# Optimization experiments

Measured on AMD Instinct MI355X. Metric: run time of the kernel, lower is better.

Reference implementation:

```python
import jax, jax.numpy as jnp
import numpy as np
import math

FS = 256
NUM_SHOT = 5


def pe_table(L, d=FS):
    pos = np.arange(L, dtype=np.float32)[:, None]
    div = np.exp(np.arange(0, d, 2, dtype=np.float32) * (-math.log(10000.0) / float(d)))
    pe = np.zeros((L, d), dtype=np.float32)
    pe[:, 0::2] = np.sin(pos * div)
    pe[:, 1::2] = np.cos(pos * div)
    return jnp.asarray(pe)


def _conv(x, w, b, stride=1):
    pad = [(1, 1), (1, 1)] if w.shape[2] == 3 else [(0, 0), (0, 0)]
    y = jax.lax.conv_general_dilated(x, w, (stride, stride), pad,
                                     dimension_numbers=('NCHW', 'OIHW', 'NCHW'))
    return y + b[None, :, None, None]


def _up2(x):
    return jnp.repeat(jnp.repeat(x, 2, axis=2), 2, axis=3)


def setup_inputs() -> dict:
    key = jax.random.key(0)
    ks = iter(jax.random.split(key, 40))
    n = lambda shape, s=0.02: jax.random.normal(next(ks), shape, dtype=jnp.float32) * s
    inp = {
        'C3': jax.random.normal(next(ks), (8, 512, 40, 40), dtype=jnp.float32),
        'C4': jax.random.normal(next(ks), (8, 1024, 20, 20), dtype=jnp.float32),
        'C5': jax.random.normal(next(ks), (8, 2048, 10, 10), dtype=jnp.float32),
        'S3': jax.random.normal(next(ks), (40, 512, 40, 40), dtype=jnp.float32),
        'S4': jax.random.normal(next(ks), (40, 1024, 20, 20), dtype=jnp.float32),
        'S5': jax.random.normal(next(ks), (40, 2048, 10, 10), dtype=jnp.float32),
        'w_p3_1': n((FS, 512, 1, 1)), 'b_p3_1': jnp.zeros((FS,), jnp.float32),
        'w_p3_2': n((FS, FS, 3, 3)), 'b_p3_2': jnp.zeros((FS,), jnp.float32),
        'w_p4_1': n((FS, 1024, 1, 1)), 'b_p4_1': jnp.zeros((FS,), jnp.float32),
        'w_p4_2': n((FS, FS, 3, 3)), 'b_p4_2': jnp.zeros((FS,), jnp.float32),
        'w_p5_1': n((FS, 2048, 1, 1)), 'b_p5_1': jnp.zeros((FS,), jnp.float32),
        'w_p5_2': n((FS, FS, 3, 3)), 'b_p5_2': jnp.zeros((FS,), jnp.float32),
        'w_p6': n((FS, 2048, 3, 3)), 'b_p6': jnp.zeros((FS,), jnp.float32),
        'w_p7': n((FS, FS, 3, 3)), 'b_p7': jnp.zeros((FS,), jnp.float32),
        'wq': n((FS, FS), 0.01), 'bq': jnp.zeros((FS,), jnp.float32),
        'wk': n((FS, FS), 0.01), 'bk': jnp.zeros((FS,), jnp.float32),
    }
    return inp


def reference(C3, C4, C5, S3, S4, S5,
              w_p3_1, b_p3_1, w_p3_2, b_p3_2,
              w_p4_1, b_p4_1, w_p4_2, b_p4_2,
              w_p5_1, b_p5_1, w_p5_2, b_p5_2,
              w_p6, b_p6, w_p7, b_p7, wq, bq, wk, bk):
    B = C3.shape[0]
    # lateral 1x1 convs (shared between query and support)
    P5x = _conv(C5, w_p5_1, b_p5_1)
    P4x = _conv(C4, w_p4_1, b_p4_1)
    P3x = _conv(C3, w_p3_1, b_p3_1)
    P5s = _conv(S5, w_p5_1, b_p5_1)
    P4s = _conv(S4, w_p4_1, b_p4_1)
    P3s = _conv(S3, w_p3_1, b_p3_1)
    # P6/P7 heads
    P6x = _conv(C5, w_p6, b_p6, stride=2)
    P7x = _conv(jax.nn.relu(P6x), w_p7, b_p7, stride=2)
    P6s = _conv(S5, w_p6, b_p6, stride=2)
    P7s = _conv(jax.nn.relu(P6s), w_p7, b_p7, stride=2)
    # query-side top-down FPN
    P4x = _up2(P5x) + P4x
    P5x2 = _conv(P5x, w_p5_2, b_p5_2)
    P3x = P3x + _up2(P4x)
    P4x2 = _conv(P4x, w_p4_2, b_p4_2)
    P3x2 = _conv(P3x, w_p3_2, b_p3_2)
    # support: [B*S, C, h, w] -> [S, B, C, h, w]
    split = lambda x: x.reshape(B, NUM_SHOT, x.shape[1], x.shape[2], x.shape[3]).transpose(1, 0, 2, 3, 4)
    q_feats = [P3x2, P4x2, P5x2, P6x, P7x]
    s_feats = [split(P3s), split(P4s), split(P5s), split(P6s), split(P7s)]
    pes = [pe_table(h * w) for h, w in [(40, 40), (20, 20), (10, 10), (5, 5), (3, 3)]]
    scale = 1.0 / math.sqrt(float(FS))
    outs = []
    for qx, sx, pe in zip(q_feats, s_feats, pes):
        _, C, H, W = qx.shape
        q = qx.reshape(B, C, H * W).transpose(0, 2, 1)                       # [B, L, C]
        s = sx.reshape(NUM_SHOT, B, C, H * W).transpose(0, 1, 3, 2) + pe      # [S, B, L, C]
        Q = q @ wq.T + bq
        K = s @ wk.T + bk
        scores = jnp.einsum('blc,sbmc->sblm', Q, K) * scale                   # [S, B, L, L]
        A = jax.nn.softmax(scores, axis=-1)
        out = jnp.einsum('sblm,sbmc->blc', A, s) / NUM_SHOT                   # shot mean
        m = out.transpose(0, 2, 1).reshape(B, C, H, W)
        outs.append(jnp.concatenate([qx, m], axis=1))
    return tuple(outs)
```

## Files before the change

kernel.cpp:

```cpp
#include <hip/hip_runtime.h>

typedef unsigned short u16;
typedef __attribute__((ext_vector_type(8))) short short8;
typedef __attribute__((ext_vector_type(4))) float floatx4;

#define DEV static __device__ __forceinline__

DEV u16 f2bf(float f) {
    union { float f; unsigned u; } v; v.f = f;
    unsigned r = v.u + 0x7fff + ((v.u >> 16) & 1);
    return (u16)(r >> 16);
}
DEV float bf2f(u16 h) {
    union { unsigned u; float f; } v; v.u = ((unsigned)h) << 16;
    return v.f;
}

DEV void load_lds16(const u16* g, u16* l) {
    __builtin_amdgcn_global_load_lds(
        (const __attribute__((address_space(1))) void*)g,
        (__attribute__((address_space(3))) void*)l, 16, 0, 0);
}

#define FLAG_BF16 1
#define FLAG_CF   2
#define FLAG_AT   4

__global__ __launch_bounds__(256, 2) void gemm_nt(
    const u16* __restrict__ A, const u16* __restrict__ BT,
    const float* __restrict__ bias,
    u16* __restrict__ obf, float* __restrict__ ocf, float* __restrict__ oat,
    int M, int K, int KS, int flags, int HW,
    long sA, long sBF, long sCF, long sAT)
{
    __shared__ u16 Al[4096];
    __shared__ u16 Bl[4096];
    const int tid = threadIdx.x, lane = tid & 63, w = tid >> 6;
    const int wr = w & 1, wc = w >> 1;
    const int col16 = lane & 15, quad = (lane >> 4) & 3;
    const int mt = blockIdx.x, nt = blockIdx.y & 1, ks = blockIdx.y >> 1, z = blockIdx.z;
    const int m0 = mt * 128, n0 = nt * 128;
    const u16* Ab = A + (size_t)z * sA;
    const int Kper = K / KS;
    const int kbeg = ks * Kper;
    const floatx4 fz = {0.f, 0.f, 0.f, 0.f};

    floatx4 acc[4][4];
#pragma unroll
    for (int i = 0; i < 4; ++i)
#pragma unroll
        for (int j = 0; j < 4; ++j) acc[i][j] = fz;

    for (int kb = 0; kb < Kper; kb += 32) {
        const int k0 = kbeg + kb;
        __syncthreads();
#pragma unroll
        for (int i = 0; i < 2; ++i) {
            int cc = w * 2 + i;
            int q = cc >> 1;
            int row = (cc & 1) * 64 + lane;
            int rg = m0 + row; rg = rg < M ? rg : (M - 1);
            load_lds16(Ab + (size_t)rg * K + k0 + q * 8, &Al[cc * 512]);
            int nr = n0 + row;
            load_lds16(BT + (size_t)nr * K + k0 + q * 8, &Bl[cc * 512]);
        }
        __syncthreads();
        short8 af[4], bfr[4];
#pragma unroll
        for (int i = 0; i < 4; ++i)
            af[i] = *(const short8*)&Al[(quad * 128 + wr * 64 + i * 16 + col16) * 8];
#pragma unroll
        for (int j = 0; j < 4; ++j)
            bfr[j] = *(const short8*)&Bl[(quad * 128 + wc * 64 + j * 16 + col16) * 8];
#pragma unroll
        for (int i = 0; i < 4; ++i)
#pragma unroll
            for (int j = 0; j < 4; ++j)
                acc[i][j] = __builtin_amdgcn_mfma_f32_16x16x32_bf16(af[i], bfr[j], acc[i][j], 0, 0, 0);
    }

#pragma unroll
    for (int j = 0; j < 4; ++j) {
        int gcol = n0 + wc * 64 + j * 16 + col16;
        float bv = (ks == 0) ? bias[gcol] : 0.f;
#pragma unroll
        for (int i = 0; i < 4; ++i) {
            int rowb = m0 + wr * 64 + i * 16 + quad * 4;
#pragma unroll
            for (int r = 0; r < 4; ++r) {
                int row = rowb + r;
                if (row < M) {
                    float v = acc[i][j][r] + bv;
                    if (flags & FLAG_BF16) obf[(size_t)z * sBF + (size_t)row * 256 + gcol] = f2bf(v);
                    if (flags & FLAG_CF)   ocf[(size_t)z * sCF + (size_t)gcol * HW + row] = v;
                    if (flags & FLAG_AT)   atomicAdd(&oat[(size_t)z * sAT + (size_t)row * 256 + gcol], v);
                }
            }
        }
    }
}

__global__ __launch_bounds__(256, 2) void flash_attn(
    const u16* __restrict__ Q,
    const u16* __restrict__ K,
    const u16* __restrict__ VT,
    float* __restrict__ outp, int L)
{
    __shared__ u16 Kl[8192];
    __shared__ u16 Vt[8192];
    __shared__ u16 Pl[4096];
    __shared__ float lrun[128];
    const int tid = threadIdx.x, lane = tid & 63, w = tid >> 6;
    const int col16 = lane & 15, quad = (lane >> 4) & 3;
    const int b = blockIdx.z, sh = blockIdx.y, sb = b * 5 + sh;
    const int q0 = blockIdx.x * 128;
    const u16* Qb = Q + (size_t)b * L * 256;
    const u16* Kb = K + (size_t)sb * L * 256;
    const u16* Vb = VT + (size_t)sb * 256 * L;
    const floatx4 fz = {0.f, 0.f, 0.f, 0.f};

    short8 qf[2][8];
#pragma unroll
    for (int lt = 0; lt < 2; ++lt) {
        int row = q0 + w * 32 + lt * 16 + col16; row = row < L ? row : (L - 1);
#pragma unroll
        for (int kc = 0; kc < 8; ++kc)
            qf[lt][kc] = *(const short8*)(Qb + (size_t)row * 256 + kc * 32 + quad * 8);
    }

    floatx4 acc[8][4];
#pragma unroll
    for (int lr = 0; lr < 8; ++lr)
#pragma unroll
        for (int ct = 0; ct < 4; ++ct) acc[lr][ct] = fz;
    float rsum[2][4] = {{0.f,0.f,0.f,0.f},{0.f,0.f,0.f,0.f}};

    const int nkt = (L + 31) >> 5;
    for (int kt = 0; kt < nkt; ++kt) {
        __syncthreads();
#pragma unroll
        for (int i = 0; i < 4; ++i) {
            int cc = w * 4 + i;
            int cg = cc * 2 + (lane >> 5);
            int row = lane & 31;
            int rg = kt * 32 + row; rg = rg < L ? rg : (L - 1);
            load_lds16(Kb + (size_t)rg * 256 + cg * 8, &Kl[cc * 512]);
            int c = cc * 16 + (lane >> 2);
            int m0 = (lane & 3) * 8;
            load_lds16(Vb + (size_t)c * L + kt * 32 + m0, &Vt[cc * 512]);
        }
        __syncthreads();
        floatx4 s00 = fz, s01 = fz, s10 = fz, s11 = fz;
#pragma unroll
        for (int kc = 0; kc < 8; ++kc) {
            short8 b0 = *(const short8*)&Kl[((kc * 4 + quad) * 32 + col16) * 8];
            short8 b1 = *(const short8*)&Kl[((kc * 4 + quad) * 32 + 16 + col16) * 8];
            s00 = __builtin_amdgcn_mfma_f32_16x16x32_bf16(qf[0][kc], b0, s00, 0, 0, 0);
            s01 = __builtin_amdgcn_mfma_f32_16x16x32_bf16(qf[0][kc], b1, s01, 0, 0, 0);
            s10 = __builtin_amdgcn_mfma_f32_16x16x32_bf16(qf[1][kc], b0, s10, 0, 0, 0);
            s11 = __builtin_amdgcn_mfma_f32_16x16x32_bf16(qf[1][kc], b1, s11, 0, 0, 0);
        }
        const bool v0 = (kt * 32 + col16) < L;
        const bool v1 = (kt * 32 + 16 + col16) < L;
        float p0[4], p1[4], p2[4], p3[4];
#pragma unroll
        for (int r = 0; r < 4; ++r) {
            p0[r] = v0 ? __expf(s00[r] * 0.0625f) : 0.f;
            p1[r] = v1 ? __expf(s01[r] * 0.0625f) : 0.f;
            p2[r] = v0 ? __expf(s10[r] * 0.0625f) : 0.f;
            p3[r] = v1 ? __expf(s11[r] * 0.0625f) : 0.f;
        }
#pragma unroll
        for (int r = 0; r < 4; ++r) {
            float v = p0[r] + p1[r];
            v += __shfl_xor(v, 1); v += __shfl_xor(v, 2); v += __shfl_xor(v, 4); v += __shfl_xor(v, 8);
            rsum[0][r] += v;
            float u = p2[r] + p3[r];
            u += __shfl_xor(u, 1); u += __shfl_xor(u, 2); u += __shfl_xor(u, 4); u += __shfl_xor(u, 8);
            rsum[1][r] += u;
        }
#pragma unroll
        for (int r = 0; r < 4; ++r) {
            int l0 = w * 32 + quad * 4 + r;
            Pl[l0 * 32 + col16]        = f2bf(p0[r]);
            Pl[l0 * 32 + 16 + col16]   = f2bf(p1[r]);
            Pl[(l0 + 16) * 32 + col16]      = f2bf(p2[r]);
            Pl[(l0 + 16) * 32 + 16 + col16] = f2bf(p3[r]);
        }
        __syncthreads();
#pragma unroll
        for (int ct = 0; ct < 4; ++ct) {
            short8 bv = *(const short8*)&Vt[(w * 64 + ct * 16 + col16) * 32 + quad * 8];
#pragma unroll
            for (int lr = 0; lr < 8; ++lr) {
                short8 ap = *(const short8*)&Pl[(lr * 16 + col16) * 32 + quad * 8];
                acc[lr][ct] = __builtin_amdgcn_mfma_f32_16x16x32_bf16(ap, bv, acc[lr][ct], 0, 0, 0);
            }
        }
    }

    if (col16 == 0) {
#pragma unroll
        for (int lt = 0; lt < 2; ++lt)
#pragma unroll
            for (int r = 0; r < 4; ++r) lrun[w * 32 + lt * 16 + quad * 4 + r] = rsum[lt][r];
    }
    __syncthreads();

#pragma unroll
    for (int lr = 0; lr < 8; ++lr) {
#pragma unroll
        for (int r = 0; r < 4; ++r) {
            int lloc = lr * 16 + quad * 4 + r;
            int l = q0 + lloc;
            if (l < L) {
                float sc = 0.2f / lrun[lloc];
#pragma unroll
                for (int ct = 0; ct < 4; ++ct) {
                    int c = w * 64 + ct * 16 + col16;
                    atomicAdd(&outp[((size_t)b * 512 + 256 + c) * L + l], acc[lr][ct][r] * sc);
                }
            }
        }
    }
}


__global__ void transp_cast(const float* __restrict__ in, u16* __restrict__ out, int C, int HW) {
    __shared__ float t[32][33];
    int z = blockIdx.z;
    int p0 = blockIdx.x * 32, c0 = blockIdx.y * 32;
    int tx = threadIdx.x & 31, ty = threadIdx.x >> 5;
    const float* ib = in + (size_t)z * C * HW;
    u16* ob = out + (size_t)z * HW * C;
#pragma unroll
    for (int i = 0; i < 4; ++i) {
        int c = c0 + ty + i * 8, p = p0 + tx;
        t[ty + i * 8][tx] = (p < HW) ? ib[(size_t)c * HW + p] : 0.f;
    }
    __syncthreads();
#pragma unroll
    for (int i = 0; i < 4; ++i) {
        int p = p0 + ty + i * 8, c = c0 + tx;
        if (p < HW) ob[(size_t)p * C + c] = f2bf(t[tx][ty + i * 8]);
    }
}

__global__ void transp_bf(const u16* __restrict__ in, u16* __restrict__ out, int L) {
    __shared__ u16 t[32][33];
    int z = blockIdx.z;
    int l0 = blockIdx.x * 32, c0 = blockIdx.y * 32;
    int tx = threadIdx.x & 31, ty = threadIdx.x >> 5;
    const u16* ib = in + (size_t)z * L * 256;
    u16* ob = out + (size_t)z * 256 * L;
#pragma unroll
    for (int i = 0; i < 4; ++i) {
        int l = l0 + ty + i * 8;
        t[ty + i * 8][tx] = (l < L) ? ib[(size_t)l * 256 + c0 + tx] : (u16)0;
    }
    __syncthreads();
#pragma unroll
    for (int i = 0; i < 4; ++i) {
        int l = l0 + tx, c = c0 + ty + i * 8;
        if (l < L) ob[(size_t)c * L + l] = t[tx][ty + i * 8];
    }
}

__global__ void cast1d(const float* __restrict__ in, u16* __restrict__ out, long n) {
    long i = (long)blockIdx.x * 256 + threadIdx.x;
    if (i < n) out[i] = f2bf(in[i]);
}

__global__ void reorder_w3(const float* __restrict__ in, u16* __restrict__ out, int C) {
    long i = (long)blockIdx.x * 256 + threadIdx.x;
    int co = (int)(i / (9L * C));
    int r = (int)(i % (9L * C));
    int t = r / C, c = r % C;
    out[i] = f2bf(in[((size_t)co * C + c) * 9 + t]);
}

__global__ void im2col_s1(const u16* __restrict__ in, u16* __restrict__ out, int H, int Wd) {
    int z = blockIdx.y, p = blockIdx.x, c = threadIdx.x;
    int y = p / Wd, x = p % Wd;
    const u16* ib = in + (size_t)z * H * Wd * 256;
    u16* ob = out + ((size_t)z * H * Wd + p) * 2304;
#pragma unroll
    for (int t = 0; t < 9; ++t) {
        int ys = y + t / 3 - 1, xs = x + t % 3 - 1;
        u16 v = 0;
        if (ys >= 0 && ys < H && xs >= 0 && xs < Wd) v = ib[((size_t)ys * Wd + xs) * 256 + c];
        ob[t * 256 + c] = v;
    }
}

__global__ void im2col_s2(const u16* __restrict__ in, u16* __restrict__ out,
                          int Hin, int Win, int Hout, int Wout, int C, int relu) {
    int z = blockIdx.y, p = blockIdx.x, tid = threadIdx.x;
    int oy = p / Wout, ox = p % Wout;
    const u16* ib = in + (size_t)z * Hin * Win * C;
    u16* ob = out + ((size_t)z * Hout * Wout + p) * (9L * C);
    for (int t = 0; t < 9; ++t) {
        int ys = oy * 2 + t / 3 - 1, xs = ox * 2 + t % 3 - 1;
        bool ok = (ys >= 0 && ys < Hin && xs >= 0 && xs < Win);
        for (int c = tid; c < C; c += 256) {
            u16 v = 0;
            if (ok) {
                v = ib[((size_t)ys * Win + xs) * C + c];
                if (relu && (v & 0x8000)) v = 0;
            }
            ob[(size_t)t * C + c] = v;
        }
    }
}

__global__ void up2add(u16* __restrict__ big, const u16* __restrict__ small, int Hb, int Wb) {
    int z = blockIdx.y, p = blockIdx.x, c = threadIdx.x;
    int y = p / Wb, x = p % Wb;
    size_t bi = ((size_t)z * Hb * Wb + p) * 256 + c;
    size_t si = ((size_t)z * (Hb / 2) * (Wb / 2) + (size_t)(y >> 1) * (Wb / 2) + (x >> 1)) * 256 + c;
    big[bi] = f2bf(bf2f(big[bi]) + bf2f(small[si]));
}

__global__ void add_pe(u16* __restrict__ s, int L) {
    int z = blockIdx.y, l = blockIdx.x, c = threadIdx.x;
    size_t i = ((size_t)z * L + l) * 256 + c;
    float arg = (float)l * expf(-0.035977892078031971f * (float)(c & ~1));
    float pe = (c & 1) ? cosf(arg) : sinf(arg);
    s[i] = f2bf(bf2f(s[i]) + pe);
}

__global__ void cast_cl(const float* __restrict__ in, u16* __restrict__ outbf,
                        float* __restrict__ doutcf, int M, int writecf) {
    int z = blockIdx.y, p = blockIdx.x, c = threadIdx.x;
    float v = in[((size_t)z * M + p) * 256 + c];
    outbf[((size_t)z * M + p) * 256 + c] = f2bf(v);
    if (writecf) doutcf[(size_t)z * 512 * M + (size_t)c * M + p] = v;
}

extern "C" void kernel_launch(void* const* d_in, const int* in_sizes, int n_in,
                              void* d_out, int out_size, void* d_ws, size_t ws_size,
                              hipStream_t stream)
{
    (void)in_sizes; (void)n_in;
    const float* C3 = (const float*)d_in[0];
    const float* C4 = (const float*)d_in[1];
    const float* C5 = (const float*)d_in[2];
    const float* S3 = (const float*)d_in[3];
    const float* S4 = (const float*)d_in[4];
    const float* S5 = (const float*)d_in[5];
    const float* w31 = (const float*)d_in[6];  const float* b31 = (const float*)d_in[7];
    const float* w32 = (const float*)d_in[8];  const float* b32 = (const float*)d_in[9];
    const float* w41 = (const float*)d_in[10]; const float* b41 = (const float*)d_in[11];
    const float* w42 = (const float*)d_in[12]; const float* b42 = (const float*)d_in[13];
    const float* w51 = (const float*)d_in[14]; const float* b51 = (const float*)d_in[15];
    const float* w52 = (const float*)d_in[16]; const float* b52 = (const float*)d_in[17];
    const float* w6  = (const float*)d_in[18]; const float* b6  = (const float*)d_in[19];
    const float* w7  = (const float*)d_in[20]; const float* b7  = (const float*)d_in[21];
    const float* wq  = (const float*)d_in[22]; const float* bq  = (const float*)d_in[23];
    const float* wk  = (const float*)d_in[24]; const float* bk  = (const float*)d_in[25];
    float* out = (float*)d_out;

    char* base = (char*)d_ws;
    size_t off = 0;
    auto alloc = [&](size_t bytes) -> void* {
        void* r = base + off;
        off = (off + bytes + 255) & ~(size_t)255;
        return r;
    };

    u16* X5t = (u16*)alloc((size_t)8  * 100  * 2048 * 2);
    u16* S5t = (u16*)alloc((size_t)40 * 100  * 2048 * 2);
    size_t alias_off = off;
    u16* X3t = (u16*)alloc((size_t)8  * 1600 * 512  * 2);
    u16* X4t = (u16*)alloc((size_t)8  * 400  * 1024 * 2);
    u16* S3t = (u16*)alloc((size_t)40 * 1600 * 512  * 2);
    u16* S4t = (u16*)alloc((size_t)40 * 400  * 1024 * 2);
    u16* imcol = (u16*)(base + alias_off);

    u16* w31b = (u16*)alloc(256L * 512 * 2);
    u16* w41b = (u16*)alloc(256L * 1024 * 2);
    u16* w51b = (u16*)alloc(256L * 2048 * 2);
    u16* wqb  = (u16*)alloc(256L * 256 * 2);
    u16* wkb  = (u16*)alloc(256L * 256 * 2);
    u16* w32b = (u16*)alloc(256L * 9 * 256 * 2);
    u16* w42b = (u16*)alloc(256L * 9 * 256 * 2);
    u16* w52b = (u16*)alloc(256L * 9 * 256 * 2);
    u16* w6b  = (u16*)alloc(256L * 9 * 2048 * 2);
    u16* w7b  = (u16*)alloc(256L * 9 * 256 * 2);

    u16* P3x = (u16*)alloc((size_t)8  * 1600 * 256 * 2);
    u16* P4x = (u16*)alloc((size_t)8  * 400  * 256 * 2);
    u16* P5x = (u16*)alloc((size_t)8  * 100  * 256 * 2);
    u16* P3s = (u16*)alloc((size_t)40 * 1600 * 256 * 2);
    u16* P4s = (u16*)alloc((size_t)40 * 400  * 256 * 2);
    u16* P5s = (u16*)alloc((size_t)40 * 100  * 256 * 2);
    u16* q3  = (u16*)alloc((size_t)8 * 1600 * 256 * 2);
    u16* q4  = (u16*)alloc((size_t)8 * 400  * 256 * 2);
    u16* q5  = (u16*)alloc((size_t)8 * 100  * 256 * 2);
    u16* q6  = (u16*)alloc((size_t)8 * 25   * 256 * 2);
    u16* q7  = (u16*)alloc((size_t)8 * 9    * 256 * 2);
    u16* P6sb = (u16*)alloc((size_t)40 * 25 * 256 * 2);
    u16* P7sb = (u16*)alloc((size_t)40 * 9  * 256 * 2);
    float* P6xf = (float*)alloc((size_t)8  * 25 * 256 * 4);
    float* P6sf = (float*)alloc((size_t)40 * 25 * 256 * 4);
    float* P7xf = (float*)alloc((size_t)8  * 9  * 256 * 4);
    float* P7sf = (float*)alloc((size_t)40 * 9  * 256 * 4);
    u16* Qb = (u16*)alloc((size_t)8  * 1600 * 256 * 2);
    u16* Kb = (u16*)alloc((size_t)40 * 1600 * 256 * 2);
    u16* sPeT = (u16*)alloc((size_t)40 * 256 * 1600 * 2 + 4096);

    if (off > ws_size) return;

    hipMemsetAsync(d_out, 0, (size_t)out_size * 4, stream);
    hipMemsetAsync(P6xf, 0, (size_t)8  * 25 * 256 * 4, stream);
    hipMemsetAsync(P6sf, 0, (size_t)40 * 25 * 256 * 4, stream);
    hipMemsetAsync(P7xf, 0, (size_t)8  * 9  * 256 * 4, stream);
    hipMemsetAsync(P7sf, 0, (size_t)40 * 9  * 256 * 4, stream);

    cast1d<<<dim3(512),  256, 0, stream>>>(w31, w31b, 256L * 512);
    cast1d<<<dim3(1024), 256, 0, stream>>>(w41, w41b, 256L * 1024);
    cast1d<<<dim3(2048), 256, 0, stream>>>(w51, w51b, 256L * 2048);
    cast1d<<<dim3(256),  256, 0, stream>>>(wq, wqb, 256L * 256);
    cast1d<<<dim3(256),  256, 0, stream>>>(wk, wkb, 256L * 256);
    reorder_w3<<<dim3(2304),  256, 0, stream>>>(w32, w32b, 256);
    reorder_w3<<<dim3(2304),  256, 0, stream>>>(w42, w42b, 256);
    reorder_w3<<<dim3(2304),  256, 0, stream>>>(w52, w52b, 256);
    reorder_w3<<<dim3(18432), 256, 0, stream>>>(w6, w6b, 2048);
    reorder_w3<<<dim3(2304),  256, 0, stream>>>(w7, w7b, 256);

    transp_cast<<<dim3(50, 16, 8),  256, 0, stream>>>(C3, X3t, 512, 1600);
    transp_cast<<<dim3(13, 32, 8),  256, 0, stream>>>(C4, X4t, 1024, 400);
    transp_cast<<<dim3(4,  64, 8),  256, 0, stream>>>(C5, X5t, 2048, 100);
    transp_cast<<<dim3(50, 16, 40), 256, 0, stream>>>(S3, S3t, 512, 1600);
    transp_cast<<<dim3(13, 32, 40), 256, 0, stream>>>(S4, S4t, 1024, 400);
    transp_cast<<<dim3(4,  64, 40), 256, 0, stream>>>(S5, S5t, 2048, 100);

    auto gemm = [&](const u16* A, const u16* BT, const float* bias,
                    u16* obf, float* ocf, float* oat,
                    int M, int K, int KS, int flags, int HW,
                    long sA, long sBF, long sCF, long sAT, int nb) {
        dim3 g((unsigned)((M + 127) / 128), (unsigned)(2 * KS), (unsigned)nb);
        gemm_nt<<<g, 256, 0, stream>>>(A, BT, bias, obf, ocf, oat, M, K, KS, flags, HW, sA, sBF, sCF, sAT);
    };

    gemm(X3t, w31b, b31, P3x, 0, 0, 1600, 512,  1, FLAG_BF16, 0, 1600L * 512,  1600L * 256, 0, 0, 8);
    gemm(X4t, w41b, b41, P4x, 0, 0, 400,  1024, 1, FLAG_BF16, 0, 400L * 1024,  400L * 256,  0, 0, 8);
    gemm(X5t, w51b, b51, P5x, 0, 0, 100,  2048, 1, FLAG_BF16, 0, 100L * 2048,  100L * 256,  0, 0, 8);
    gemm(S3t, w31b, b31, P3s, 0, 0, 1600, 512,  1, FLAG_BF16, 0, 1600L * 512,  1600L * 256, 0, 0, 40);
    gemm(S4t, w41b, b41, P4s, 0, 0, 400,  1024, 1, FLAG_BF16, 0, 400L * 1024,  400L * 256,  0, 0, 40);
    gemm(S5t, w51b, b51, P5s, 0, 0, 100,  2048, 1, FLAG_BF16, 0, 100L * 2048,  100L * 256,  0, 0, 40);

    const size_t lvl_off[5] = {0, 6553600, 8192000, 8601600, 8704000};

    im2col_s2<<<dim3(25, 8), 256, 0, stream>>>(X5t, imcol, 10, 10, 5, 5, 2048, 0);
    gemm(imcol, w6b, b6, 0, 0, P6xf, 25, 18432, 8, FLAG_AT, 0, 25L * 18432, 0, 0, 25L * 256, 8);
    im2col_s2<<<dim3(25, 40), 256, 0, stream>>>(S5t, imcol, 10, 10, 5, 5, 2048, 0);
    gemm(imcol, w6b, b6, 0, 0, P6sf, 25, 18432, 8, FLAG_AT, 0, 25L * 18432, 0, 0, 25L * 256, 40);
    cast_cl<<<dim3(25, 8),  256, 0, stream>>>(P6xf, q6, out + lvl_off[3], 25, 1);
    cast_cl<<<dim3(25, 40), 256, 0, stream>>>(P6sf, P6sb, 0, 25, 0);
    im2col_s2<<<dim3(9, 8), 256, 0, stream>>>(q6, imcol, 5, 5, 3, 3, 256, 1);
    gemm(imcol, w7b, b7, 0, 0, P7xf, 9, 2304, 4, FLAG_AT, 0, 9L * 2304, 0, 0, 9L * 256, 8);
    im2col_s2<<<dim3(9, 40), 256, 0, stream>>>(P6sb, imcol, 5, 5, 3, 3, 256, 1);
    gemm(imcol, w7b, b7, 0, 0, P7sf, 9, 2304, 4, FLAG_AT, 0, 9L * 2304, 0, 0, 9L * 256, 40);
    cast_cl<<<dim3(9, 8),  256, 0, stream>>>(P7xf, q7, out + lvl_off[4], 9, 1);
    cast_cl<<<dim3(9, 40), 256, 0, stream>>>(P7sf, P7sb, 0, 9, 0);

    up2add<<<dim3(400, 8),  256, 0, stream>>>(P4x, P5x, 20, 20);
    up2add<<<dim3(1600, 8), 256, 0, stream>>>(P3x, P4x, 40, 40);

    im2col_s1<<<dim3(100, 8), 256, 0, stream>>>(P5x, imcol, 10, 10);
    gemm(imcol, w52b, b52, q5, out + lvl_off[2], 0, 100, 2304, 1, FLAG_BF16 | FLAG_CF, 100,
         100L * 2304, 100L * 256, 512L * 100, 0, 8);
    im2col_s1<<<dim3(400, 8), 256, 0, stream>>>(P4x, imcol, 20, 20);
    gemm(imcol, w42b, b42, q4, out + lvl_off[1], 0, 400, 2304, 1, FLAG_BF16 | FLAG_CF, 400,
         400L * 2304, 400L * 256, 512L * 400, 0, 8);
    im2col_s1<<<dim3(1600, 8), 256, 0, stream>>>(P3x, imcol, 40, 40);
    gemm(imcol, w32b, b32, q3, out + lvl_off[0], 0, 1600, 2304, 1, FLAG_BF16 | FLAG_CF, 1600,
         1600L * 2304, 1600L * 256, 512L * 1600, 0, 8);

    const int Ls[5] = {1600, 400, 100, 25, 9};
    u16* qbuf[5] = {q3, q4, q5, q6, q7};
    u16* sbuf[5] = {P3s, P4s, P5s, P6sb, P7sb};
    for (int lv = 0; lv < 5; ++lv) {
        int L = Ls[lv];
        add_pe<<<dim3(L, 40), 256, 0, stream>>>(sbuf[lv], L);
        transp_bf<<<dim3((L + 31) / 32, 8, 40), 256, 0, stream>>>(sbuf[lv], sPeT, L);
        gemm(qbuf[lv], wqb, bq, Qb, 0, 0, L, 256, 1, FLAG_BF16, 0, (long)L * 256, (long)L * 256, 0, 0, 8);
        gemm(sbuf[lv], wkb, bk, Kb, 0, 0, L, 256, 1, FLAG_BF16, 0, (long)L * 256, (long)L * 256, 0, 0, 40);
        flash_attn<<<dim3((L + 127) / 128, 5, 8), 256, 0, stream>>>(Qb, Kb, sPeT, out + lvl_off[lv], L);
    }
}
```

Measured before the change: 2.333 ms.

## Replace fused flash attention with materialized exp-score GEMMs and batched flat GEMMs

```diff
diff --git a/kernel.cpp b/kernel.cpp
--- a/kernel.cpp
+++ b/kernel.cpp
@@ -23,15 +23,15 @@
 }
 
 #define FLAG_BF16 1
-#define FLAG_CF   2
 #define FLAG_AT   4
+#define FLAG_PV   8
 
 __global__ __launch_bounds__(256, 2) void gemm_nt(
     const u16* __restrict__ A, const u16* __restrict__ BT,
     const float* __restrict__ bias,
-    u16* __restrict__ obf, float* __restrict__ ocf, float* __restrict__ oat,
-    int M, int K, int KS, int flags, int HW,
-    long sA, long sBF, long sCF, long sAT)
+    u16* __restrict__ obf, float* __restrict__ oat, const float* __restrict__ lsum,
+    int M, int K, int KS, int flags, int zoff,
+    long sA, long sBT, long sBF, long sAT)
 {
     __shared__ u16 Al[4096];
     __shared__ u16 Bl[4096];
@@ -39,8 +39,10 @@
     const int wr = w & 1, wc = w >> 1;
     const int col16 = lane & 15, quad = (lane >> 4) & 3;
     const int mt = blockIdx.x, nt = blockIdx.y & 1, ks = blockIdx.y >> 1, z = blockIdx.z;
+    const int sb = zoff + z;
     const int m0 = mt * 128, n0 = nt * 128;
     const u16* Ab = A + (size_t)z * sA;
+    const u16* Bb = BT + (size_t)sb * sBT;
     const int Kper = K / KS;
     const int kbeg = ks * Kper;
     const floatx4 fz = {0.f, 0.f, 0.f, 0.f};
@@ -62,7 +64,7 @@
             int rg = m0 + row; rg = rg < M ? rg : (M - 1);
             load_lds16(Ab + (size_t)rg * K + k0 + q * 8, &Al[cc * 512]);
             int nr = n0 + row;
-            load_lds16(BT + (size_t)nr * K + k0 + q * 8, &Bl[cc * 512]);
+            load_lds16(Bb + (size_t)nr * K + k0 + q * 8, &Bl[cc * 512]);
         }
         __syncthreads();
         short8 af[4], bfr[4];
@@ -82,7 +84,7 @@
 #pragma unroll
     for (int j = 0; j < 4; ++j) {
         int gcol = n0 + wc * 64 + j * 16 + col16;
-        float bv = (ks == 0) ? bias[gcol] : 0.f;
+        float bv = (bias && ks == 0) ? bias[gcol] : 0.f;
 #pragma unroll
         for (int i = 0; i < 4; ++i) {
             int rowb = m0 + wr * 64 + i * 16 + quad * 4;
@@ -92,135 +94,88 @@
                 if (row < M) {
                     float v = acc[i][j][r] + bv;
                     if (flags & FLAG_BF16) obf[(size_t)z * sBF + (size_t)row * 256 + gcol] = f2bf(v);
-                    if (flags & FLAG_CF)   ocf[(size_t)z * sCF + (size_t)gcol * HW + row] = v;
                     if (flags & FLAG_AT)   atomicAdd(&oat[(size_t)z * sAT + (size_t)row * 256 + gcol], v);
+                    if (flags & FLAG_PV) {
+                        int bl = z / 5;
+                        float sc = 0.2f / lsum[(size_t)sb * 1664 + row];
+                        atomicAdd(&oat[(size_t)bl * sAT + (size_t)row * 256 + gcol], v * sc);
+                    }
                 }
             }
         }
     }
 }
 
-__global__ __launch_bounds__(256, 2) void flash_attn(
-    const u16* __restrict__ Q,
-    const u16* __restrict__ K,
-    const u16* __restrict__ VT,
-    float* __restrict__ outp, int L)
+__global__ __launch_bounds__(256, 2) void gemm_qk_exp(
+    const u16* __restrict__ Q, const u16* __restrict__ Km,
+    u16* __restrict__ eS, float* __restrict__ lsum,
+    int M, int Kpad, int zoff)
 {
-    __shared__ u16 Kl[8192];
-    __shared__ u16 Vt[8192];
-    __shared__ u16 Pl[4096];
-    __shared__ float lrun[128];
+    __shared__ u16 Al[4096];
+    __shared__ u16 Bl[4096];
     const int tid = threadIdx.x, lane = tid & 63, w = tid >> 6;
+    const int wr = w & 1, wc = w >> 1;
     const int col16 = lane & 15, quad = (lane >> 4) & 3;
-    const int b = blockIdx.z, sh = blockIdx.y, sb = b * 5 + sh;
-    const int q0 = blockIdx.x * 128;
-    const u16* Qb = Q + (size_t)b * L * 256;
-    const u16* Kb = K + (size_t)sb * L * 256;
-    const u16* Vb = VT + (size_t)sb * 256 * L;
+    const int mt = blockIdx.x, nt = blockIdx.y, z = blockIdx.z;
+    const int sb = zoff + z;
+    const int m0 = mt * 128, n0 = nt * 128;
+    const u16* Ab = Q + (size_t)(sb / 5) * M * 256;
+    const u16* Bb = Km + (size_t)sb * M * 256;
+    u16* eSb = eS + (size_t)z * M * Kpad;
     const floatx4 fz = {0.f, 0.f, 0.f, 0.f};
 
-    short8 qf[2][8];
-#pragma unroll
-    for (int lt = 0; lt < 2; ++lt) {
-        int row = q0 + w * 32 + lt * 16 + col16; row = row < L ? row : (L - 1);
-#pragma unroll
-        for (int kc = 0; kc < 8; ++kc)
-            qf[lt][kc] = *(const short8*)(Qb + (size_t)row * 256 + kc * 32 + quad * 8);
-    }
-
-    floatx4 acc[8][4];
-#pragma unroll
-    for (int lr = 0; lr < 8; ++lr)
-#pragma unroll
-        for (int ct = 0; ct < 4; ++ct) acc[lr][ct] = fz;
-    float rsum[2][4] = {{0.f,0.f,0.f,0.f},{0.f,0.f,0.f,0.f}};
-
-    const int nkt = (L + 31) >> 5;
-    for (int kt = 0; kt < nkt; ++kt) {
+    floatx4 acc[4][4];
+#pragma unroll
+    for (int i = 0; i < 4; ++i)
+#pragma unroll
+        for (int j = 0; j < 4; ++j) acc[i][j] = fz;
+
+    for (int k0 = 0; k0 < 256; k0 += 32) {
         __syncthreads();
 #pragma unroll
-        for (int i = 0; i < 4; ++i) {
-            int cc = w * 4 + i;
-            int cg = cc * 2 + (lane >> 5);
-            int row = lane & 31;
-            int rg = kt * 32 + row; rg = rg < L ? rg : (L - 1);
-            load_lds16(Kb + (size_t)rg * 256 + cg * 8, &Kl[cc * 512]);
-            int c = cc * 16 + (lane >> 2);
-            int m0 = (lane & 3) * 8;
-            load_lds16(Vb + (size_t)c * L + kt * 32 + m0, &Vt[cc * 512]);
+        for (int i = 0; i < 2; ++i) {
+            int cc = w * 2 + i;
+            int q = cc >> 1;
+            int row = (cc & 1) * 64 + lane;
+            int rg = m0 + row; rg = rg < M ? rg : (M - 1);
+            load_lds16(Ab + (size_t)rg * 256 + k0 + q * 8, &Al[cc * 512]);
+            int nr = n0 + row; nr = nr < M ? nr : (M - 1);
+            load_lds16(Bb + (size_t)nr * 256 + k0 + q * 8, &Bl[cc * 512]);
         }
         __syncthreads();
-        floatx4 s00 = fz, s01 = fz, s10 = fz, s11 = fz;
-#pragma unroll
-        for (int kc = 0; kc < 8; ++kc) {
-            short8 b0 = *(const short8*)&Kl[((kc * 4 + quad) * 32 + col16) * 8];
-            short8 b1 = *(const short8*)&Kl[((kc * 4 + quad) * 32 + 16 + col16) * 8];
-            s00 = __builtin_amdgcn_mfma_f32_16x16x32_bf16(qf[0][kc], b0, s00, 0, 0, 0);
-            s01 = __builtin_amdgcn_mfma_f32_16x16x32_bf16(qf[0][kc], b1, s01, 0, 0, 0);
-            s10 = __builtin_amdgcn_mfma_f32_16x16x32_bf16(qf[1][kc], b0, s10, 0, 0, 0);
-            s11 = __builtin_amdgcn_mfma_f32_16x16x32_bf16(qf[1][kc], b1, s11, 0, 0, 0);
-        }
-        const bool v0 = (kt * 32 + col16) < L;
-        const bool v1 = (kt * 32 + 16 + col16) < L;
-        float p0[4], p1[4], p2[4], p3[4];
+        short8 af[4], bfr[4];
+#pragma unroll
+        for (int i = 0; i < 4; ++i)
+            af[i] = *(const short8*)&Al[(quad * 128 + wr * 64 + i * 16 + col16) * 8];
+#pragma unroll
+        for (int j = 0; j < 4; ++j)
+            bfr[j] = *(const short8*)&Bl[(quad * 128 + wc * 64 + j * 16 + col16) * 8];
+#pragma unroll
+        for (int i = 0; i < 4; ++i)
+#pragma unroll
+            for (int j = 0; j < 4; ++j)
+                acc[i][j] = __builtin_amdgcn_mfma_f32_16x16x32_bf16(af[i], bfr[j], acc[i][j], 0, 0, 0);
+    }
+
+#pragma unroll
+    for (int i = 0; i < 4; ++i) {
 #pragma unroll
         for (int r = 0; r < 4; ++r) {
-            p0[r] = v0 ? __expf(s00[r] * 0.0625f) : 0.f;
-            p1[r] = v1 ? __expf(s01[r] * 0.0625f) : 0.f;
-            p2[r] = v0 ? __expf(s10[r] * 0.0625f) : 0.f;
-            p3[r] = v1 ? __expf(s11[r] * 0.0625f) : 0.f;
-        }
-#pragma unroll
-        for (int r = 0; r < 4; ++r) {
-            float v = p0[r] + p1[r];
-            v += __shfl_xor(v, 1); v += __shfl_xor(v, 2); v += __shfl_xor(v, 4); v += __shfl_xor(v, 8);
-            rsum[0][r] += v;
-            float u = p2[r] + p3[r];
-            u += __shfl_xor(u, 1); u += __shfl_xor(u, 2); u += __shfl_xor(u, 4); u += __shfl_xor(u, 8);
-            rsum[1][r] += u;
-        }
-#pragma unroll
-        for (int r = 0; r < 4; ++r) {
-            int l0 = w * 32 + quad * 4 + r;
-            Pl[l0 * 32 + col16]        = f2bf(p0[r]);
-            Pl[l0 * 32 + 16 + col16]   = f2bf(p1[r]);
-            Pl[(l0 + 16) * 32 + col16]      = f2bf(p2[r]);
-            Pl[(l0 + 16) * 32 + 16 + col16] = f2bf(p3[r]);
-        }
-        __syncthreads();
-#pragma unroll
-        for (int ct = 0; ct < 4; ++ct) {
-            short8 bv = *(const short8*)&Vt[(w * 64 + ct * 16 + col16) * 32 + quad * 8];
-#pragma unroll
-            for (int lr = 0; lr < 8; ++lr) {
-                short8 ap = *(const short8*)&Pl[(lr * 16 + col16) * 32 + quad * 8];
-                acc[lr][ct] = __builtin_amdgcn_mfma_f32_16x16x32_bf16(ap, bv, acc[lr][ct], 0, 0, 0);
+            int row = m0 + wr * 64 + i * 16 + quad * 4 + r;
+            float s = 0.f;
+#pragma unroll
+            for (int j = 0; j < 4; ++j) {
+                int gcol = n0 + wc * 64 + j * 16 + col16;
+                float v = 0.f;
+                if (row < M && gcol < M) v = __expf(acc[i][j][r] * 0.0625f);
+                u16 h = f2bf(v);
+                if (row < M) eSb[(size_t)row * Kpad + gcol] = h;
+                s += bf2f(h);
             }
-        }
-    }
-
-    if (col16 == 0) {
-#pragma unroll
-        for (int lt = 0; lt < 2; ++lt)
-#pragma unroll
-            for (int r = 0; r < 4; ++r) lrun[w * 32 + lt * 16 + quad * 4 + r] = rsum[lt][r];
-    }
-    __syncthreads();
-
-#pragma unroll
-    for (int lr = 0; lr < 8; ++lr) {
-#pragma unroll
-        for (int r = 0; r < 4; ++r) {
-            int lloc = lr * 16 + quad * 4 + r;
-            int l = q0 + lloc;
-            if (l < L) {
-                float sc = 0.2f / lrun[lloc];
-#pragma unroll
-                for (int ct = 0; ct < 4; ++ct) {
-                    int c = w * 64 + ct * 16 + col16;
-                    atomicAdd(&outp[((size_t)b * 512 + 256 + c) * L + l], acc[lr][ct][r] * sc);
-                }
-            }
+            s += __shfl_xor(s, 1); s += __shfl_xor(s, 2);
+            s += __shfl_xor(s, 4); s += __shfl_xor(s, 8);
+            if ((lane & 15) == 0 && row < M)
+                atomicAdd(&lsum[(size_t)sb * 1664 + row], s);
         }
     }
 }
@@ -246,13 +201,13 @@
     }
 }
 
-__global__ void transp_bf(const u16* __restrict__ in, u16* __restrict__ out, int L) {
+__global__ void transp_bf(const u16* __restrict__ in, u16* __restrict__ out, int L, int Kpad) {
     __shared__ u16 t[32][33];
     int z = blockIdx.z;
     int l0 = blockIdx.x * 32, c0 = blockIdx.y * 32;
     int tx = threadIdx.x & 31, ty = threadIdx.x >> 5;
     const u16* ib = in + (size_t)z * L * 256;
-    u16* ob = out + (size_t)z * 256 * L;
+    u16* ob = out + (size_t)z * 256 * Kpad;
 #pragma unroll
     for (int i = 0; i < 4; ++i) {
         int l = l0 + ty + i * 8;
@@ -262,7 +217,7 @@
 #pragma unroll
     for (int i = 0; i < 4; ++i) {
         int l = l0 + tx, c = c0 + ty + i * 8;
-        if (l < L) ob[(size_t)c * L + l] = t[tx][ty + i * 8];
+        ob[(size_t)c * Kpad + l] = t[tx][ty + i * 8];
     }
 }
 
@@ -329,12 +284,27 @@
     s[i] = f2bf(bf2f(s[i]) + pe);
 }
 
-__global__ void cast_cl(const float* __restrict__ in, u16* __restrict__ outbf,
-                        float* __restrict__ doutcf, int M, int writecf) {
-    int z = blockIdx.y, p = blockIdx.x, c = threadIdx.x;
-    float v = in[((size_t)z * M + p) * 256 + c];
-    outbf[((size_t)z * M + p) * 256 + c] = f2bf(v);
-    if (writecf) doutcf[(size_t)z * 512 * M + (size_t)c * M + p] = v;
+__global__ void cast_store(const float* __restrict__ in, u16* __restrict__ qout,
+                           float* __restrict__ dout, int M, int choff) {
+    __shared__ float t[32][33];
+    int z = blockIdx.z, p0 = blockIdx.x * 32, c0 = blockIdx.y * 32;
+    int tx = threadIdx.x & 31, ty = threadIdx.x >> 5;
+#pragma unroll
+    for (int i = 0; i < 4; ++i) {
+        int p = p0 + ty + i * 8, c = c0 + tx;
+        float v = 0.f;
+        if (p < M) v = in[((size_t)z * M + p) * 256 + c];
+        t[ty + i * 8][tx] = v;
+        if (qout && p < M) qout[((size_t)z * M + p) * 256 + c] = f2bf(v);
+    }
+    __syncthreads();
+    if (dout) {
+#pragma unroll
+        for (int i = 0; i < 4; ++i) {
+            int p = p0 + tx, c = c0 + ty + i * 8;
+            if (p < M) dout[((size_t)z * 512 + choff + c) * M + p] = t[tx][ty + i * 8];
+        }
+    }
 }
 
 extern "C" void kernel_launch(void* const* d_in, const int* in_sizes, int n_in,
@@ -368,14 +338,18 @@
         return r;
     };
 
-    u16* X5t = (u16*)alloc((size_t)8  * 100  * 2048 * 2);
-    u16* S5t = (u16*)alloc((size_t)40 * 100  * 2048 * 2);
-    size_t alias_off = off;
-    u16* X3t = (u16*)alloc((size_t)8  * 1600 * 512  * 2);
-    u16* X4t = (u16*)alloc((size_t)8  * 400  * 1024 * 2);
-    u16* S3t = (u16*)alloc((size_t)40 * 1600 * 512  * 2);
-    u16* S4t = (u16*)alloc((size_t)40 * 400  * 1024 * 2);
-    u16* imcol = (u16*)(base + alias_off);
+    char* arena = (char*)alloc(117964800);
+    u16* X3t = (u16*)(arena + 0);
+    u16* X4t = (u16*)(arena + 13107200);
+    u16* S3t = (u16*)(arena + 19660800);
+    u16* S4t = (u16*)(arena + 85196800);
+    u16*   imcol   = (u16*)(arena + 0);
+    float* convf32 = (float*)(arena + 58982400);
+    u16*   expS    = (u16*)(arena + 0);
+    float* attnf32 = (float*)(arena + 106496000);
+
+    u16* X5t = (u16*)alloc((size_t)8  * 100 * 2048 * 2);
+    u16* S5t = (u16*)alloc((size_t)40 * 100 * 2048 * 2);
 
     u16* w31b = (u16*)alloc(256L * 512 * 2);
     u16* w41b = (u16*)alloc(256L * 1024 * 2);
@@ -405,9 +379,10 @@
     float* P6sf = (float*)alloc((size_t)40 * 25 * 256 * 4);
     float* P7xf = (float*)alloc((size_t)8  * 9  * 256 * 4);
     float* P7sf = (float*)alloc((size_t)40 * 9  * 256 * 4);
-    u16* Qb = (u16*)alloc((size_t)8  * 1600 * 256 * 2);
-    u16* Kb = (u16*)alloc((size_t)40 * 1600 * 256 * 2);
-    u16* sPeT = (u16*)alloc((size_t)40 * 256 * 1600 * 2 + 4096);
+    u16* Qb   = (u16*)alloc((size_t)8  * 1600 * 256 * 2);
+    u16* Kb   = (u16*)alloc((size_t)40 * 1600 * 256 * 2);
+    u16* sPeT = (u16*)alloc((size_t)40 * 256 * 1664 * 2);
+    float* lsum = (float*)alloc((size_t)40 * 1664 * 4);
 
     if (off > ws_size) return;
 
@@ -436,57 +411,75 @@
     transp_cast<<<dim3(4,  64, 40), 256, 0, stream>>>(S5, S5t, 2048, 100);
 
     auto gemm = [&](const u16* A, const u16* BT, const float* bias,
-                    u16* obf, float* ocf, float* oat,
-                    int M, int K, int KS, int flags, int HW,
-                    long sA, long sBF, long sCF, long sAT, int nb) {
-        dim3 g((unsigned)((M + 127) / 128), (unsigned)(2 * KS), (unsigned)nb);
-        gemm_nt<<<g, 256, 0, stream>>>(A, BT, bias, obf, ocf, oat, M, K, KS, flags, HW, sA, sBF, sCF, sAT);
+                    u16* obf, float* oat, const float* ls,
+                    int M, int K, int KS, int flags, int zoff,
+                    long sA, long sBT, long sBF, long sAT, int nbz) {
+        dim3 g((unsigned)((M + 127) / 128), (unsigned)(2 * KS), (unsigned)nbz);
+        gemm_nt<<<g, 256, 0, stream>>>(A, BT, bias, obf, oat, ls, M, K, KS, flags, zoff,
+                                       sA, sBT, sBF, sAT);
     };
 
-    gemm(X3t, w31b, b31, P3x, 0, 0, 1600, 512,  1, FLAG_BF16, 0, 1600L * 512,  1600L * 256, 0, 0, 8);
-    gemm(X4t, w41b, b41, P4x, 0, 0, 400,  1024, 1, FLAG_BF16, 0, 400L * 1024,  400L * 256,  0, 0, 8);
-    gemm(X5t, w51b, b51, P5x, 0, 0, 100,  2048, 1, FLAG_BF16, 0, 100L * 2048,  100L * 256,  0, 0, 8);
-    gemm(S3t, w31b, b31, P3s, 0, 0, 1600, 512,  1, FLAG_BF16, 0, 1600L * 512,  1600L * 256, 0, 0, 40);
-    gemm(S4t, w41b, b41, P4s, 0, 0, 400,  1024, 1, FLAG_BF16, 0, 400L * 1024,  400L * 256,  0, 0, 40);
-    gemm(S5t, w51b, b51, P5s, 0, 0, 100,  2048, 1, FLAG_BF16, 0, 100L * 2048,  100L * 256,  0, 0, 40);
+    gemm(X3t, w31b, b31, P3x, 0, 0, 12800, 512,  1, FLAG_BF16, 0, 0, 0, 0, 0, 1);
+    gemm(X4t, w41b, b41, P4x, 0, 0, 3200,  1024, 1, FLAG_BF16, 0, 0, 0, 0, 0, 1);
+    gemm(X5t, w51b, b51, P5x, 0, 0, 800,   2048, 1, FLAG_BF16, 0, 0, 0, 0, 0, 1);
+    gemm(S3t, w31b, b31, P3s, 0, 0, 64000, 512,  1, FLAG_BF16, 0, 0, 0, 0, 0, 1);
+    gemm(S4t, w41b, b41, P4s, 0, 0, 16000, 1024, 1, FLAG_BF16, 0, 0, 0, 0, 0, 1);
+    gemm(S5t, w51b, b51, P5s, 0, 0, 4000,  2048, 1, FLAG_BF16, 0, 0, 0, 0, 0, 1);
 
     const size_t lvl_off[5] = {0, 6553600, 8192000, 8601600, 8704000};
 
     im2col_s2<<<dim3(25, 8), 256, 0, stream>>>(X5t, imcol, 10, 10, 5, 5, 2048, 0);
-    gemm(imcol, w6b, b6, 0, 0, P6xf, 25, 18432, 8, FLAG_AT, 0, 25L * 18432, 0, 0, 25L * 256, 8);
+    gemm(imcol, w6b, b6, 0, P6xf, 0, 200, 18432, 8, FLAG_AT, 0, 0, 0, 0, 0, 1);
     im2col_s2<<<dim3(25, 40), 256, 0, stream>>>(S5t, imcol, 10, 10, 5, 5, 2048, 0);
-    gemm(imcol, w6b, b6, 0, 0, P6sf, 25, 18432, 8, FLAG_AT, 0, 25L * 18432, 0, 0, 25L * 256, 40);
-    cast_cl<<<dim3(25, 8),  256, 0, stream>>>(P6xf, q6, out + lvl_off[3], 25, 1);
-    cast_cl<<<dim3(25, 40), 256, 0, stream>>>(P6sf, P6sb, 0, 25, 0);
+    gemm(imcol, w6b, b6, 0, P6sf, 0, 1000, 18432, 8, FLAG_AT, 0, 0, 0, 0, 0, 1);
+    cast_store<<<dim3(1, 8, 8),  256, 0, stream>>>(P6xf, q6, out + lvl_off[3], 25, 0);
+    cast_store<<<dim3(1, 8, 40), 256, 0, stream>>>(P6sf, P6sb, 0, 25, 0);
     im2col_s2<<<dim3(9, 8), 256, 0, stream>>>(q6, imcol, 5, 5, 3, 3, 256, 1);
-    gemm(imcol, w7b, b7, 0, 0, P7xf, 9, 2304, 4, FLAG_AT, 0, 9L * 2304, 0, 0, 9L * 256, 8);
+    gemm(imcol, w7b, b7, 0, P7xf, 0, 72, 2304, 4, FLAG_AT, 0, 0, 0, 0, 0, 1);
     im2col_s2<<<dim3(9, 40), 256, 0, stream>>>(P6sb, imcol, 5, 5, 3, 3, 256, 1);
-    gemm(imcol, w7b, b7, 0, 0, P7sf, 9, 2304, 4, FLAG_AT, 0, 9L * 2304, 0, 0, 9L * 256, 40);
-    cast_cl<<<dim3(9, 8),  256, 0, stream>>>(P7xf, q7, out + lvl_off[4], 9, 1);
-    cast_cl<<<dim3(9, 40), 256, 0, stream>>>(P7sf, P7sb, 0, 9, 0);
+    gemm(imcol, w7b, b7, 0, P7sf, 0, 360, 2304, 4, FLAG_AT, 0, 0, 0, 0, 0, 1);
+    cast_store<<<dim3(1, 8, 8),  256, 0, stream>>>(P7xf, q7, out + lvl_off[4], 9, 0);
+    cast_store<<<dim3(1, 8, 40), 256, 0, stream>>>(P7sf, P7sb, 0, 9, 0);
 
     up2add<<<dim3(400, 8),  256, 0, stream>>>(P4x, P5x, 20, 20);
     up2add<<<dim3(1600, 8), 256, 0, stream>>>(P3x, P4x, 40, 40);
 
     im2col_s1<<<dim3(100, 8), 256, 0, stream>>>(P5x, imcol, 10, 10);
-    gemm(imcol, w52b, b52, q5, out + lvl_off[2], 0, 100, 2304, 1, FLAG_BF16 | FLAG_CF, 100,
-         100L * 2304, 100L * 256, 512L * 100, 0, 8);
+    hipMemsetAsync(convf32, 0, (size_t)8 * 100 * 256 * 4, stream);
+    gemm(imcol, w52b, b52, 0, convf32, 0, 800, 2304, 4, FLAG_AT, 0, 0, 0, 0, 0, 1);
+    cast_store<<<dim3(4, 8, 8), 256, 0, stream>>>(convf32, q5, out + lvl_off[2], 100, 0);
+
     im2col_s1<<<dim3(400, 8), 256, 0, stream>>>(P4x, imcol, 20, 20);
-    gemm(imcol, w42b, b42, q4, out + lvl_off[1], 0, 400, 2304, 1, FLAG_BF16 | FLAG_CF, 400,
-         400L * 2304, 400L * 256, 512L * 400, 0, 8);
+    hipMemsetAsync(convf32, 0, (size_t)8 * 400 * 256 * 4, stream);
+    gemm(imcol, w42b, b42, 0, convf32, 0, 3200, 2304, 4, FLAG_AT, 0, 0, 0, 0, 0, 1);
+    cast_store<<<dim3(13, 8, 8), 256, 0, stream>>>(convf32, q4, out + lvl_off[1], 400, 0);
+
     im2col_s1<<<dim3(1600, 8), 256, 0, stream>>>(P3x, imcol, 40, 40);
-    gemm(imcol, w32b, b32, q3, out + lvl_off[0], 0, 1600, 2304, 1, FLAG_BF16 | FLAG_CF, 1600,
-         1600L * 2304, 1600L * 256, 512L * 1600, 0, 8);
-
-    const int Ls[5] = {1600, 400, 100, 25, 9};
+    hipMemsetAsync(convf32, 0, (size_t)8 * 1600 * 256 * 4, stream);
+    gemm(imcol, w32b, b32, 0, convf32, 0, 12800, 2304, 4, FLAG_AT, 0, 0, 0, 0, 0, 1);
+    cast_store<<<dim3(50, 8, 8), 256, 0, stream>>>(convf32, q3, out + lvl_off[0], 1600, 0);
+
+    const int Ls[5]    = {1600, 400, 100, 25, 9};
+    const int Kpads[5] = {1664, 512, 128, 128, 128};
     u16* qbuf[5] = {q3, q4, q5, q6, q7};
     u16* sbuf[5] = {P3s, P4s, P5s, P6sb, P7sb};
     for (int lv = 0; lv < 5; ++lv) {
-        int L = Ls[lv];
+        int L = Ls[lv], Kpad = Kpads[lv];
         add_pe<<<dim3(L, 40), 256, 0, stream>>>(sbuf[lv], L);
-        transp_bf<<<dim3((L + 31) / 32, 8, 40), 256, 0, stream>>>(sbuf[lv], sPeT, L);
-        gemm(qbuf[lv], wqb, bq, Qb, 0, 0, L, 256, 1, FLAG_BF16, 0, (long)L * 256, (long)L * 256, 0, 0, 8);
-        gemm(sbuf[lv], wkb, bk, Kb, 0, 0, L, 256, 1, FLAG_BF16, 0, (long)L * 256, (long)L * 256, 0, 0, 40);
-        flash_attn<<<dim3((L + 127) / 128, 5, 8), 256, 0, stream>>>(Qb, Kb, sPeT, out + lvl_off[lv], L);
-    }
-}
+        transp_bf<<<dim3(Kpad / 32, 8, 40), 256, 0, stream>>>(sbuf[lv], sPeT, L, Kpad);
+        gemm(qbuf[lv], wqb, bq, Qb, 0, 0, 8 * L,  256, 1, FLAG_BF16, 0, 0, 0, 0, 0, 1);
+        gemm(sbuf[lv], wkb, bk, Kb, 0, 0, 40 * L, 256, 1, FLAG_BF16, 0, 0, 0, 0, 0, 1);
+        hipMemsetAsync(lsum, 0, (size_t)40 * 1664 * 4, stream);
+        int chunk = (lv == 0) ? 20 : 40;
+        for (int c0 = 0; c0 < 40; c0 += chunk) {
+            int nb = chunk / 5;
+            hipMemsetAsync(attnf32, 0, (size_t)nb * L * 256 * 4, stream);
+            dim3 gq((unsigned)((L + 127) / 128), (unsigned)(Kpad / 128), (unsigned)chunk);
+            gemm_qk_exp<<<gq, 256, 0, stream>>>(Qb, Kb, expS, lsum, L, Kpad, c0);
+            gemm(expS, sPeT, 0, 0, attnf32, lsum, L, Kpad, 1, FLAG_PV, c0,
+                 (long)L * Kpad, (long)256 * Kpad, 0, (long)L * 256, chunk);
+            cast_store<<<dim3((L + 31) / 32, 8, nb), 256, 0, stream>>>(
+                attnf32, 0, out + lvl_off[lv] + (size_t)(c0 / 5) * 512 * L, L, 256);
+        }
+    }
+}
```

After: 2.321 ms. About the same (-0.5%).
